# Kernel optimization log

Measured on AMD Instinct MI355X. Metric: run time of the kernel, lower is better.

Reference implementation:

```python
import jax, jax.numpy as jnp
import numpy as np

EMBED_DIM = 1024
NUM_HEADS = 16
HEAD_DIM = EMBED_DIM // NUM_HEADS
KERNEL = 3
PAD = KERNEL // 2
B, L = 4, 1024


def conv1d(x, w, b):
    # x: [B, D, L], w: [D_out, D_in, K], b: [D_out]; 'same' padding like nn.Conv1d(padding=K//2)
    y = jax.lax.conv_general_dilated(
        x, w, window_strides=(1,), padding=[(PAD, PAD)],
        dimension_numbers=('NCH', 'OIH', 'NCH'))
    return y + b[None, :, None]


def setup_inputs() -> dict:
    key = jax.random.key(0)
    ks = jax.random.split(key, 12)
    fan = EMBED_DIM * KERNEL
    bound = 1.0 / np.sqrt(fan)
    def wconv(k):
        return jax.random.uniform(k, (EMBED_DIM, EMBED_DIM, KERNEL), jnp.float32, -bound, bound)
    def bconv(k):
        return jax.random.uniform(k, (EMBED_DIM,), jnp.float32, -bound, bound)
    return {
        'query': jax.random.normal(ks[0], (B, L, EMBED_DIM), jnp.float32),
        'key': jax.random.normal(ks[1], (B, L, EMBED_DIM), jnp.float32),
        'value': jax.random.normal(ks[2], (B, L, EMBED_DIM), jnp.float32),
        'key_padding_mask': jax.random.randint(ks[3], (B, L), 0, 2) > 0,
        'attn_mask': jnp.zeros((L, L), jnp.float32),
        'q_w': wconv(ks[4]), 'q_b': bconv(ks[5]),
        'k_w': wconv(ks[6]), 'k_b': bconv(ks[7]),
        'v_w': wconv(ks[8]), 'v_b': bconv(ks[9]),
        'o_w': wconv(ks[10]), 'o_b': bconv(ks[11]),
    }


def reference(query, key, value, key_padding_mask, attn_mask,
              q_w, q_b, k_w, k_b, v_w, v_b, o_w, o_b):
    scale = HEAD_DIM ** -0.5
    # projections: [B, D, L]
    q = conv1d(jnp.swapaxes(query, 1, 2), q_w, q_b)
    k = conv1d(jnp.swapaxes(key, 1, 2), k_w, k_b)
    v = conv1d(jnp.swapaxes(value, 1, 2), v_w, v_b)
    # [B, H, d, L]
    q = q.reshape(B, NUM_HEADS, HEAD_DIM, L)
    k = k.reshape(B, NUM_HEADS, HEAD_DIM, L)
    v = v.reshape(B, NUM_HEADS, HEAD_DIM, L)
    # scores: [B, H, L, L]
    scores = jnp.einsum('bhdi,bhdj->bhij', q, k) * scale
    scores = scores + attn_mask[None, None, :, :]
    scores = jnp.where(key_padding_mask[:, None, None, :], -jnp.inf, scores)
    attn = jax.nn.softmax(scores, axis=-1)  # dropout p=0 (eval) -> identity
    out = jnp.einsum('bhij,bhdj->bhdi', attn, v)  # [B, H, d, L]
    out = out.reshape(B, EMBED_DIM, L)
    out = conv1d(out, o_w, o_b)
    return jnp.swapaxes(out, 1, 2)  # [B, L, D]
```

## Files before the change

kernel.cpp:

```cpp
#include <hip/hip_runtime.h>
#include <math.h>

#define NB 4
#define NL 1024
#define ND 1024
#define NH 16
#define HD 64

typedef __attribute__((ext_vector_type(8))) short bf16x8;
typedef __attribute__((ext_vector_type(4))) float f32x4;

static __device__ __forceinline__ unsigned short f32_to_bf16(float f) {
  unsigned u = __float_as_uint(f);
  u += 0x7FFFu + ((u >> 16) & 1u);
  return (unsigned short)(u >> 16);
}
static __device__ __forceinline__ float bf16_to_f32(unsigned short s) {
  return __uint_as_float(((unsigned)s) << 16);
}
static __device__ __forceinline__ void split1(float x, unsigned short* h, unsigned short* l) {
  unsigned u = __float_as_uint(x);
  *h = (unsigned short)(u >> 16);
  float r = x - __uint_as_float(u & 0xFFFF0000u);
  *l = (unsigned short)(__float_as_uint(r) >> 16);
}
static __device__ __forceinline__ void split8(float4 a, float4 b, bf16x8* hi, bf16x8* lo) {
  unsigned u[8] = {__float_as_uint(a.x), __float_as_uint(a.y),
                   __float_as_uint(a.z), __float_as_uint(a.w),
                   __float_as_uint(b.x), __float_as_uint(b.y),
                   __float_as_uint(b.z), __float_as_uint(b.w)};
  union { unsigned p[4]; bf16x8 v; } H, L;
#pragma unroll
  for (int p = 0; p < 4; ++p) {
    unsigned u0 = u[2 * p], u1 = u[2 * p + 1];
    H.p[p] = __builtin_amdgcn_perm(u1, u0, 0x07060302u);
    unsigned l0 = __float_as_uint(__uint_as_float(u0) - __uint_as_float(u0 & 0xFFFF0000u));
    unsigned l1 = __float_as_uint(__uint_as_float(u1) - __uint_as_float(u1 & 0xFFFF0000u));
    L.p[p] = __builtin_amdgcn_perm(l1, l0, 0x07060302u);
  }
  *hi = H.v; *lo = L.v;
}

__global__ __launch_bounds__(256) void wcvt_kernel(
    const float* __restrict__ w0, const float* __restrict__ w1,
    const float* __restrict__ w2, const float* __restrict__ w3,
    unsigned short* __restrict__ wb, int* __restrict__ flag)
{
  if (blockIdx.x == 0 && blockIdx.y == 0 && threadIdx.x == 0) flag[0] = 0;
  const int t = blockIdx.y;
  const int o = blockIdx.x;
  const float* w = (t == 0) ? w0 : (t == 1) ? w1 : (t == 2) ? w2 : w3;
  unsigned short* hi = wb + (size_t)t * 6 * (1u << 20);
  unsigned short* lo = hi + 3 * (1u << 20);
  const int tid = threadIdx.x;
  float v[12];
  const float* src = w + (size_t)o * (ND * 3) + tid * 12;
#pragma unroll
  for (int j = 0; j < 3; ++j) {
    float4 f = *(const float4*)(src + j * 4);
    v[j * 4 + 0] = f.x; v[j * 4 + 1] = f.y; v[j * 4 + 2] = f.z; v[j * 4 + 3] = f.w;
  }
#pragma unroll
  for (int k = 0; k < 3; ++k) {
    unsigned short hh[4], ll[4];
#pragma unroll
    for (int ii = 0; ii < 4; ++ii) {
      float x = v[ii * 3 + k];
      unsigned short h = f32_to_bf16(x);
      float r = x - bf16_to_f32(h);
      hh[ii] = h; ll[ii] = f32_to_bf16(r);
    }
    size_t dst = (size_t)k * (ND * ND) + (size_t)o * ND + tid * 4;
    *(ushort4*)&hi[dst] = make_ushort4(hh[0], hh[1], hh[2], hh[3]);
    *(ushort4*)&lo[dst] = make_ushort4(ll[0], ll[1], ll[2], ll[3]);
  }
}

__global__ __launch_bounds__(256) void amask_scan(
    const float* __restrict__ a, int* __restrict__ flag)
{
  size_t i = ((size_t)blockIdx.x * 256 + threadIdx.x) * 4;
  float4 v = *(const float4*)&a[i];
  if (v.x != 0.f || v.y != 0.f || v.z != 0.f || v.w != 0.f) atomicOr(flag, 1);
}

template <int MODE>
__global__ __launch_bounds__(256, 3) void conv_mfma5(
    const float* __restrict__ X0, const float* __restrict__ X1,
    const float* __restrict__ X2,
    const unsigned short* __restrict__ wb,
    const float* b0, const float* b1, const float* b2,
    unsigned short* qh, unsigned short* ql,
    unsigned short* kh, unsigned short* kl, unsigned short* vv,
    float* P)
{
  __shared__ __align__(16) float Af[4096];
  __shared__ __align__(16) unsigned short Bh[4096];
  __shared__ __align__(16) unsigned short Bl[4096];

  const int tid = threadIdx.x, lane = tid & 63, wave = tid >> 6;
  const int lin = blockIdx.x + 8 * (blockIdx.y + 32 * blockIdx.z);
  const int g = lin & 7, t = lin >> 3;
  const int nb = (g & 3) * 2 + (t & 1);
  const int mb = (g >> 2) * 16 + ((t >> 1) & 15);
  const int z  = t >> 5;
  const int n0 = nb * 128, m0 = mb * 128;
  const int b = m0 >> 10, l0v = m0 & (NL - 1);

  const unsigned short* Wh = (MODE == 0) ? wb + (size_t)z * 6 * (1u << 20) : wb;
  const unsigned short* Wl = Wh + 3 * (1u << 20);
  const float* X = (MODE == 0) ? (z == 0 ? X0 : (z == 1 ? X1 : X2)) : X0;

  const int wm = (wave >> 1) * 64, wn = (wave & 1) * 64;
  const int mrow = lane & 15, quad = lane >> 4;
  const int r16 = lane >> 2, cs = lane & 3;
  const int src_chunk = (cs - (r16 >> 1)) & 3;
  const int bswz = ((quad + (mrow >> 1)) & 3) * 8;

  f32x4 acc[4][4] = {};
  const int NS = (MODE == 0) ? 96 : 32;

  auto stage = [&](int s) {
    const int koff = (MODE == 0) ? (s >> 5) : z;
    const int i0 = (s & 31) * 32;
#pragma unroll
    for (int j = 0; j < 2; ++j) {
      const int seg = wave * 2 + j;
      const size_t gw = ((size_t)koff << 20) +
                        (size_t)(n0 + seg * 16 + r16) * ND + i0 + src_chunk * 8;
      __builtin_amdgcn_global_load_lds(
          (const __attribute__((address_space(1))) unsigned int*)(Wh + gw),
          (__attribute__((address_space(3))) unsigned int*)&Bh[seg * 512], 16, 0, 0);
      __builtin_amdgcn_global_load_lds(
          (const __attribute__((address_space(1))) unsigned int*)(Wl + gw),
          (__attribute__((address_space(3))) unsigned int*)&Bl[seg * 512], 16, 0, 0);
    }
#pragma unroll
    for (int j = 0; j < 4; ++j) {
      const int sl = (wave * 4 + j) * 64 + lane;
      const int row = sl >> 3, sir = sl & 7;
      const int chunk = (sir - (row & 7)) & 7;
      const float* gp;
      if (MODE == 0) {
        int l = l0v + row + koff - 1;
        l = (l < 0) ? 0 : (l > NL - 1 ? NL - 1 : l);
        gp = X + ((size_t)(b << 10) + l) * ND + i0 + chunk * 4;
      } else {
        gp = X + (size_t)(b * 1026 + l0v + z + row) * ND + i0 + chunk * 4;
      }
      __builtin_amdgcn_global_load_lds(
          (const __attribute__((address_space(1))) unsigned int*)gp,
          (__attribute__((address_space(3))) unsigned int*)&Af[(wave * 4 + j) * 256],
          16, 0, 0);
    }
  };

  bf16x8 ah[4], al[4], bh[4], bl[4];
  auto readfrags = [&]() {
#pragma unroll
    for (int mi = 0; mi < 4; ++mi) {
      const int row = wm + mi * 16 + mrow, r7 = row & 7;
      float4 fa = *(const float4*)&Af[row * 32 + (((quad * 2) + r7) & 7) * 4];
      float4 fb = *(const float4*)&Af[row * 32 + (((quad * 2 + 1) + r7) & 7) * 4];
      split8(fa, fb, &ah[mi], &al[mi]);
    }
#pragma unroll
    for (int ni = 0; ni < 4; ++ni) {
      const int brow = wn + ni * 16 + mrow;
      bh[ni] = *(const bf16x8*)&Bh[brow * 32 + bswz];
      bl[ni] = *(const bf16x8*)&Bl[brow * 32 + bswz];
    }
  };

  auto edgefix = [&](int s) {
    if (MODE == 0) {
      const int koff = s >> 5;
      const bool e_lo = (l0v == 0 && koff == 0);
      const bool e_hi = (l0v == NL - 128 && koff == 2);
      if (e_lo || e_hi) {
        const int er = e_lo ? 0 : 127;
        if (tid < 8) *(float4*)&Af[er * 32 + tid * 4] = make_float4(0.f, 0.f, 0.f, 0.f);
        __syncthreads();
      }
    }
  };

  stage(0);
  __syncthreads();
  edgefix(0);
  readfrags();

  for (int s = 0; s < NS; ++s) {
    __syncthreads();
    if (s + 1 < NS) stage(s + 1);
#pragma unroll
    for (int ni = 0; ni < 4; ++ni)
#pragma unroll
      for (int mi = 0; mi < 4; ++mi) {
        acc[mi][ni] = __builtin_amdgcn_mfma_f32_16x16x32_bf16(ah[mi], bh[ni], acc[mi][ni], 0, 0, 0);
        acc[mi][ni] = __builtin_amdgcn_mfma_f32_16x16x32_bf16(ah[mi], bl[ni], acc[mi][ni], 0, 0, 0);
        acc[mi][ni] = __builtin_amdgcn_mfma_f32_16x16x32_bf16(al[mi], bh[ni], acc[mi][ni], 0, 0, 0);
      }
    __syncthreads();
    if (s + 1 < NS) { edgefix(s + 1); readfrags(); }
  }

  if (MODE == 0) {
    const float* bias = (z == 0) ? b0 : (z == 1) ? b1 : b2;
#pragma unroll
    for (int ni = 0; ni < 4; ++ni) {
      const int n = n0 + wn + ni * 16 + mrow;
      const float bv = bias[n];
      const int h2 = n >> 6, dd = n & 63;
#pragma unroll
      for (int mi = 0; mi < 4; ++mi) {
        const int mbase = m0 + wm + mi * 16 + quad * 4;
        f32x4 v = acc[mi][ni];
#pragma unroll
        for (int r = 0; r < 4; ++r) {
          const int l = (mbase + r) & (NL - 1);
          const size_t o = (((size_t)b * NH + h2) * NL + l) * HD + dd;
          float val = v[r] + bv;
          if (z == 0) {
            val *= 0.125f;
            unsigned short hs, ls; split1(val, &hs, &ls);
            qh[o] = hs; ql[o] = ls;
          } else if (z == 1) {
            unsigned short hs, ls; split1(val, &hs, &ls);
            kh[o] = hs; kl[o] = ls;
          } else {
            vv[o] = f32_to_bf16(val);
          }
        }
      }
    }
  } else {
    float* Pz = P + (size_t)z * ((size_t)NB * NL * ND);
#pragma unroll
    for (int ni = 0; ni < 4; ++ni) {
      const int n = n0 + wn + ni * 16 + mrow;
#pragma unroll
      for (int mi = 0; mi < 4; ++mi) {
        const int mbase = m0 + wm + mi * 16 + quad * 4;
        f32x4 v = acc[mi][ni];
#pragma unroll
        for (int r = 0; r < 4; ++r) {
          const int l = (mbase + r) & (NL - 1);
          Pz[((size_t)(b << 10) + l) * ND + n] = v[r];
        }
      }
    }
  }
}

__global__ __launch_bounds__(256) void reduce_kernel(
    const float* __restrict__ P, const float* __restrict__ bias, float* __restrict__ out)
{
  const size_t S = (size_t)NB * NL * ND;
  const size_t idx = ((size_t)blockIdx.x * 256 + threadIdx.x) * 4;
  const int n = (int)(idx & (ND - 1));
  float4 p0 = *(const float4*)&P[idx];
  float4 p1 = *(const float4*)&P[idx + S];
  float4 p2 = *(const float4*)&P[idx + 2 * S];
  float4 bv = *(const float4*)&bias[n];
  float4 r;
  r.x = p0.x + p1.x + p2.x + bv.x;
  r.y = p0.y + p1.y + p2.y + bv.y;
  r.z = p0.z + p1.z + p2.z + bv.z;
  r.w = p0.w + p1.w + p2.w + bv.w;
  *(float4*)&out[idx] = r;
}

__global__ __launch_bounds__(256, 3) void attn_mfma3(
    const unsigned short* __restrict__ qhp, const unsigned short* __restrict__ qlp,
    const unsigned short* __restrict__ khp, const unsigned short* __restrict__ klp,
    const unsigned short* __restrict__ vvp, const int* __restrict__ kpm,
    const float* __restrict__ amask, const int* __restrict__ aflagp,
    float* __restrict__ AO)
{
  __shared__ __align__(16) unsigned short SM[8192 + 4608];
  unsigned short* Kh = SM;
  unsigned short* Kl = SM + 4096;
  unsigned short* Vt = SM + 8192;

  const int tid = threadIdx.x, lane = tid & 63, wave = tid >> 6;
  const int c = lane & 15, quad = lane >> 4;
  const int lin = blockIdx.x;
  const int bh_ = (lin & 7) + 8 * (lin >> 7);
  const int mt = (lin >> 3) & 15;
  const int b = bh_ >> 4, h = bh_ & 15;
  const int m0 = mt * 64;
  const size_t base = (size_t)bh_ * (NL * HD);
  const int aflag = *aflagp;
  const int mrow = wave * 16 + c;
  const int gm = m0 + mrow;

  if (h == 0 && mt == 0)
    *(float4*)&AO[(size_t)(b * 1026) * ND + tid * 4] = make_float4(0.f, 0.f, 0.f, 0.f);
  if (h == 0 && mt == 15)
    *(float4*)&AO[((size_t)(b * 1026) + 1025) * ND + tid * 4] = make_float4(0.f, 0.f, 0.f, 0.f);

  const int rowo = lane >> 3;
  const int grano = ((lane & 7) - rowo) & 7;

#pragma unroll
  for (int j = 0; j < 2; ++j) {
    const int s = wave * 2 + j;
    const size_t go = base + (size_t)(m0 + s * 8 + rowo) * HD + grano * 8;
    __builtin_amdgcn_global_load_lds(
        (const __attribute__((address_space(1))) unsigned int*)(qhp + go),
        (__attribute__((address_space(3))) unsigned int*)&Kh[s * 512], 16, 0, 0);
    __builtin_amdgcn_global_load_lds(
        (const __attribute__((address_space(1))) unsigned int*)(qlp + go),
        (__attribute__((address_space(3))) unsigned int*)&Kl[s * 512], 16, 0, 0);
  }
  __syncthreads();
  bf16x8 qbh[2], qbl[2];
#pragma unroll
  for (int kb = 0; kb < 2; ++kb) {
    const int cso = ((kb * 4 + quad + mrow) & 7) * 8;
    qbh[kb] = *(const bf16x8*)&Kh[mrow * 64 + cso];
    qbl[kb] = *(const bf16x8*)&Kl[mrow * 64 + cso];
  }

  f32x4 acc[4] = {};
  float m_r = -INFINITY, l_r = 0.0f;
  const int sr = tid >> 2, scq = tid & 3;

  for (int n0t = 0; n0t < NL; n0t += 64) {
    __syncthreads();

    float mval[4][4];
#pragma unroll
    for (int nf = 0; nf < 4; ++nf) {
      int4 pm4 = *(const int4*)&kpm[b * NL + n0t + nf * 16 + quad * 4];
      const int* pmi = &pm4.x;
#pragma unroll
      for (int r = 0; r < 4; ++r) {
        float am = 0.f;
        if (aflag) am = amask[(size_t)gm * NL + (n0t + nf * 16 + quad * 4 + r)];
        mval[nf][r] = pmi[r] ? -INFINITY : am;
      }
    }

#pragma unroll
    for (int j = 0; j < 2; ++j) {
      const int s = wave * 2 + j;
      const size_t go = base + (size_t)(n0t + s * 8 + rowo) * HD + grano * 8;
      __builtin_amdgcn_global_load_lds(
          (const __attribute__((address_space(1))) unsigned int*)(khp + go),
          (__attribute__((address_space(3))) unsigned int*)&Kh[s * 512], 16, 0, 0);
      __builtin_amdgcn_global_load_lds(
          (const __attribute__((address_space(1))) unsigned int*)(klp + go),
          (__attribute__((address_space(3))) unsigned int*)&Kl[s * 512], 16, 0, 0);
    }
#pragma unroll
    for (int ii = 0; ii < 2; ++ii) {
      const int c8 = scq * 2 + ii;
      uint4 u = *(const uint4*)(vvp + base + (size_t)(n0t + sr) * HD + c8 * 8);
      const unsigned short* pe = (const unsigned short*)&u;
#pragma unroll
      for (int e = 0; e < 8; ++e) {
        const int dd = c8 * 8 + e;
        Vt[dd * 72 + (((sr >> 3) + dd) & 7) * 8 + (sr & 7)] = pe[e];
      }
    }
    __syncthreads();

    f32x4 sa[4] = {};
#pragma unroll
    for (int kb = 0; kb < 2; ++kb)
#pragma unroll
      for (int nf = 0; nf < 4; ++nf) {
        const int row = nf * 16 + c;
        const int cso = ((kb * 4 + quad + row) & 7) * 8;
        bf16x8 kah = *(const bf16x8*)&Kh[row * 64 + cso];
        bf16x8 kal = *(const bf16x8*)&Kl[row * 64 + cso];
        sa[nf] = __builtin_amdgcn_mfma_f32_16x16x32_bf16(kah, qbh[kb], sa[nf], 0, 0, 0);
        sa[nf] = __builtin_amdgcn_mfma_f32_16x16x32_bf16(kah, qbl[kb], sa[nf], 0, 0, 0);
        sa[nf] = __builtin_amdgcn_mfma_f32_16x16x32_bf16(kal, qbh[kb], sa[nf], 0, 0, 0);
      }

    float p[4][4];
    float tmax = -INFINITY;
#pragma unroll
    for (int nf = 0; nf < 4; ++nf)
#pragma unroll
      for (int r = 0; r < 4; ++r) {
        float s = sa[nf][r] + mval[nf][r];
        p[nf][r] = s;
        tmax = fmaxf(tmax, s);
      }
    tmax = fmaxf(tmax, __shfl_xor(tmax, 16));
    tmax = fmaxf(tmax, __shfl_xor(tmax, 32));
    const float newm = fmaxf(m_r, tmax);
    const float msafe = (newm == -INFINITY) ? 0.f : newm;
    const float alpha = __expf(m_r - msafe);
    float rs = 0.f;
#pragma unroll
    for (int nf = 0; nf < 4; ++nf)
#pragma unroll
      for (int r = 0; r < 4; ++r) {
        float e = __expf(p[nf][r] - msafe);
        p[nf][r] = e;
        rs += e;
      }
    rs += __shfl_xor(rs, 16);
    rs += __shfl_xor(rs, 32);
    l_r = l_r * alpha + rs;
    m_r = newm;
#pragma unroll
    for (int df = 0; df < 4; ++df) {
      acc[df][0] *= alpha; acc[df][1] *= alpha;
      acc[df][2] *= alpha; acc[df][3] *= alpha;
    }

    unsigned q16[4][2];
#pragma unroll
    for (int nf = 0; nf < 4; ++nf)
#pragma unroll
      for (int w = 0; w < 2; ++w)
        q16[nf][w] = (unsigned)f32_to_bf16(p[nf][2 * w]) |
                     ((unsigned)f32_to_bf16(p[nf][2 * w + 1]) << 16);
#pragma unroll
    for (int kb = 0; kb < 2; ++kb) {
      union { unsigned d[4]; bf16x8 v; } pb;
#pragma unroll
      for (int w = 0; w < 4; ++w) {
        const int addr = ((((quad & 1) * 2 + (w >> 1)) * 16 + c) << 2);
        unsigned v0 = __builtin_amdgcn_ds_bpermute(addr, (int)q16[2 * kb][w & 1]);
        unsigned v1 = __builtin_amdgcn_ds_bpermute(addr, (int)q16[2 * kb + 1][w & 1]);
        pb.d[w] = (quad >> 1) ? v1 : v0;
      }
#pragma unroll
      for (int df = 0; df < 4; ++df) {
        const int row = df * 16 + c;
        const int cso = ((kb * 4 + quad + row) & 7) * 8;
        bf16x8 va = *(const bf16x8*)&Vt[row * 72 + cso];
        acc[df] = __builtin_amdgcn_mfma_f32_16x16x32_bf16(va, pb.v, acc[df], 0, 0, 0);
      }
    }
  }

  __syncthreads();
  const float inv = 1.0f / l_r;
  float* Ob = (float*)SM + wave * (16 * 68);
#pragma unroll
  for (int df = 0; df < 4; ++df)
#pragma unroll
    for (int r = 0; r < 4; ++r)
      Ob[c * 68 + df * 16 + quad * 4 + r] = acc[df][r] * inv;
  __syncthreads();
  const int mr2 = lane >> 2, cq2 = lane & 3;
#pragma unroll
  for (int ii = 0; ii < 4; ++ii) {
    const int chunk = cq2 * 4 + ii;
    float4 v = *(const float4*)&Ob[mr2 * 68 + chunk * 4];
    *(float4*)&AO[((size_t)(b * 1026) + (m0 + wave * 16 + mr2) + 1) * ND +
                  h * HD + chunk * 4] = v;
  }
}

extern "C" void kernel_launch(void* const* d_in, const int* in_sizes, int n_in,
                              void* d_out, int out_size, void* d_ws, size_t ws_size,
                              hipStream_t stream) {
  (void)in_sizes; (void)n_in; (void)out_size; (void)ws_size;
  const float* query = (const float*)d_in[0];
  const float* key_  = (const float*)d_in[1];
  const float* value = (const float*)d_in[2];
  const int*   kpm   = (const int*)d_in[3];
  const float* amask = (const float*)d_in[4];
  const float* q_w = (const float*)d_in[5];
  const float* q_b = (const float*)d_in[6];
  const float* k_w = (const float*)d_in[7];
  const float* k_b = (const float*)d_in[8];
  const float* v_w = (const float*)d_in[9];
  const float* v_b = (const float*)d_in[10];
  const float* o_w = (const float*)d_in[11];
  const float* o_b = (const float*)d_in[12];
  float* out = (float*)d_out;

  const size_t WB_BYTES = 50331648;
  unsigned short* Wb = (unsigned short*)d_ws;
  unsigned short* qh = (unsigned short*)((char*)d_ws + WB_BYTES);
  unsigned short* ql = qh + 4194304;
  unsigned short* kh = ql + 4194304;
  unsigned short* kl = kh + 4194304;
  unsigned short* vv = kl + 4194304;
  float* AO = (float*)d_ws;
  float* P  = (float*)((char*)d_ws + WB_BYTES);
  int* flag = (int*)d_out;

  wcvt_kernel<<<dim3(1024, 4), 256, 0, stream>>>(q_w, k_w, v_w, o_w, Wb, flag);
  amask_scan<<<1024, 256, 0, stream>>>(amask, flag);
  conv_mfma5<0><<<dim3(8, 32, 3), 256, 0, stream>>>(
      query, key_, value, Wb, q_b, k_b, v_b, qh, ql, kh, kl, vv, nullptr);
  attn_mfma3<<<1024, 256, 0, stream>>>(qh, ql, kh, kl, vv, kpm, amask, flag, AO);
  conv_mfma5<1><<<dim3(8, 32, 3), 256, 0, stream>>>(
      AO, nullptr, nullptr, Wb + (size_t)3 * 6 * (1u << 20),
      nullptr, nullptr, nullptr, nullptr, nullptr, nullptr, nullptr, nullptr, P);
  reduce_kernel<<<4096, 256, 0, stream>>>(P, o_b, out);
}
```

Baseline: 523.2 us.

## Switch conv GEMM to 32x32x16 MFMA and drop software prefetch of fragments

Replaces the 16x16x32 bf16 MFMA tiling in the conv projection kernel with 32x32x16 MFMA, so each wave holds a 2x2 grid of 32x32 accumulator tiles and issues fewer, larger instructions with fewer LDS fragment reads per FLOP. The loop is also restructured: it no longer stages the next K-slice while computing the current one, and instead loads, syncs, reads fragments and computes in sequence. The larger tiles are meant to cut LDS traffic and instruction overhead, but removing the overlap between global loads and MFMA work may expose memory latency. Epilogue index mapping is updated to the 32x32 accumulator layout.

```diff
diff --git a/kernel.cpp b/kernel.cpp
--- a/kernel.cpp
+++ b/kernel.cpp
@@ -9,6 +9,7 @@
 
 typedef __attribute__((ext_vector_type(8))) short bf16x8;
 typedef __attribute__((ext_vector_type(4))) float f32x4;
+typedef __attribute__((ext_vector_type(16))) float f32x16;
 
 static __device__ __forceinline__ unsigned short f32_to_bf16(float f) {
   unsigned u = __float_as_uint(f);
@@ -85,7 +86,7 @@
 }
 
 template <int MODE>
-__global__ __launch_bounds__(256, 3) void conv_mfma5(
+__global__ __launch_bounds__(256, 3) void conv_mfma6(
     const float* __restrict__ X0, const float* __restrict__ X1,
     const float* __restrict__ X2,
     const unsigned short* __restrict__ wb,
@@ -111,13 +112,12 @@
   const unsigned short* Wl = Wh + 3 * (1u << 20);
   const float* X = (MODE == 0) ? (z == 0 ? X0 : (z == 1 ? X1 : X2)) : X0;
 
-  const int wm = (wave >> 1) * 64, wn = (wave & 1) * 64;
-  const int mrow = lane & 15, quad = lane >> 4;
+  const int wm2 = (wave >> 1) * 64, wn2 = (wave & 1) * 64;
+  const int ln31 = lane & 31, khalf = lane >> 5;
   const int r16 = lane >> 2, cs = lane & 3;
   const int src_chunk = (cs - (r16 >> 1)) & 3;
-  const int bswz = ((quad + (mrow >> 1)) & 3) * 8;
-
-  f32x4 acc[4][4] = {};
+
+  f32x16 acc[2][2] = {};
   const int NS = (MODE == 0) ? 96 : 32;
 
   auto stage = [&](int s) {
@@ -155,23 +155,6 @@
     }
   };
 
-  bf16x8 ah[4], al[4], bh[4], bl[4];
-  auto readfrags = [&]() {
-#pragma unroll
-    for (int mi = 0; mi < 4; ++mi) {
-      const int row = wm + mi * 16 + mrow, r7 = row & 7;
-      float4 fa = *(const float4*)&Af[row * 32 + (((quad * 2) + r7) & 7) * 4];
-      float4 fb = *(const float4*)&Af[row * 32 + (((quad * 2 + 1) + r7) & 7) * 4];
-      split8(fa, fb, &ah[mi], &al[mi]);
-    }
-#pragma unroll
-    for (int ni = 0; ni < 4; ++ni) {
-      const int brow = wn + ni * 16 + mrow;
-      bh[ni] = *(const bf16x8*)&Bh[brow * 32 + bswz];
-      bl[ni] = *(const bf16x8*)&Bl[brow * 32 + bswz];
-    }
-  };
-
   auto edgefix = [&](int s) {
     if (MODE == 0) {
       const int koff = s >> 5;
@@ -185,42 +168,57 @@
     }
   };
 
-  stage(0);
-  __syncthreads();
-  edgefix(0);
-  readfrags();
-
   for (int s = 0; s < NS; ++s) {
+    stage(s);
     __syncthreads();
-    if (s + 1 < NS) stage(s + 1);
-#pragma unroll
-    for (int ni = 0; ni < 4; ++ni)
-#pragma unroll
-      for (int mi = 0; mi < 4; ++mi) {
-        acc[mi][ni] = __builtin_amdgcn_mfma_f32_16x16x32_bf16(ah[mi], bh[ni], acc[mi][ni], 0, 0, 0);
-        acc[mi][ni] = __builtin_amdgcn_mfma_f32_16x16x32_bf16(ah[mi], bl[ni], acc[mi][ni], 0, 0, 0);
-        acc[mi][ni] = __builtin_amdgcn_mfma_f32_16x16x32_bf16(al[mi], bh[ni], acc[mi][ni], 0, 0, 0);
+    edgefix(s);
+
+    bf16x8 ah[2][2], al[2][2];
+#pragma unroll
+    for (int mf = 0; mf < 2; ++mf) {
+      const int row = wm2 + mf * 32 + ln31, r7 = row & 7;
+#pragma unroll
+      for (int ts = 0; ts < 2; ++ts) {
+        const int c0 = ts * 4 + khalf * 2;
+        float4 fa = *(const float4*)&Af[row * 32 + (((c0 + 0) + r7) & 7) * 4];
+        float4 fb = *(const float4*)&Af[row * 32 + (((c0 + 1) + r7) & 7) * 4];
+        split8(fa, fb, &ah[mf][ts], &al[mf][ts]);
+      }
+    }
+#pragma unroll
+    for (int ts = 0; ts < 2; ++ts)
+#pragma unroll
+      for (int nf = 0; nf < 2; ++nf) {
+        const int brow = wn2 + nf * 32 + ln31;
+        const int slot = ((ts * 2 + khalf) + ((brow & 15) >> 1)) & 3;
+        bf16x8 bhf = *(const bf16x8*)&Bh[brow * 32 + slot * 8];
+        bf16x8 blf = *(const bf16x8*)&Bl[brow * 32 + slot * 8];
+#pragma unroll
+        for (int mf = 0; mf < 2; ++mf) {
+          acc[mf][nf] = __builtin_amdgcn_mfma_f32_32x32x16_bf16(ah[mf][ts], bhf, acc[mf][nf], 0, 0, 0);
+          acc[mf][nf] = __builtin_amdgcn_mfma_f32_32x32x16_bf16(ah[mf][ts], blf, acc[mf][nf], 0, 0, 0);
+          acc[mf][nf] = __builtin_amdgcn_mfma_f32_32x32x16_bf16(al[mf][ts], bhf, acc[mf][nf], 0, 0, 0);
+        }
       }
     __syncthreads();
-    if (s + 1 < NS) { edgefix(s + 1); readfrags(); }
   }
 
   if (MODE == 0) {
     const float* bias = (z == 0) ? b0 : (z == 1) ? b1 : b2;
 #pragma unroll
-    for (int ni = 0; ni < 4; ++ni) {
-      const int n = n0 + wn + ni * 16 + mrow;
+    for (int nf = 0; nf < 2; ++nf) {
+      const int n = n0 + wn2 + nf * 32 + ln31;
       const float bv = bias[n];
       const int h2 = n >> 6, dd = n & 63;
 #pragma unroll
-      for (int mi = 0; mi < 4; ++mi) {
-        const int mbase = m0 + wm + mi * 16 + quad * 4;
-        f32x4 v = acc[mi][ni];
-#pragma unroll
-        for (int r = 0; r < 4; ++r) {
-          const int l = (mbase + r) & (NL - 1);
+      for (int mf = 0; mf < 2; ++mf) {
+        f32x16 v = acc[mf][nf];
+#pragma unroll
+        for (int reg = 0; reg < 16; ++reg) {
+          const int mloc = (reg & 3) + 8 * (reg >> 2) + 4 * khalf;
+          const int l = l0v + wm2 + mf * 32 + mloc;
           const size_t o = (((size_t)b * NH + h2) * NL + l) * HD + dd;
-          float val = v[r] + bv;
+          float val = v[reg] + bv;
           if (z == 0) {
             val *= 0.125f;
             unsigned short hs, ls; split1(val, &hs, &ls);
@@ -237,16 +235,16 @@
   } else {
     float* Pz = P + (size_t)z * ((size_t)NB * NL * ND);
 #pragma unroll
-    for (int ni = 0; ni < 4; ++ni) {
-      const int n = n0 + wn + ni * 16 + mrow;
-#pragma unroll
-      for (int mi = 0; mi < 4; ++mi) {
-        const int mbase = m0 + wm + mi * 16 + quad * 4;
-        f32x4 v = acc[mi][ni];
-#pragma unroll
-        for (int r = 0; r < 4; ++r) {
-          const int l = (mbase + r) & (NL - 1);
-          Pz[((size_t)(b << 10) + l) * ND + n] = v[r];
+    for (int nf = 0; nf < 2; ++nf) {
+      const int n = n0 + wn2 + nf * 32 + ln31;
+#pragma unroll
+      for (int mf = 0; mf < 2; ++mf) {
+        f32x16 v = acc[mf][nf];
+#pragma unroll
+        for (int reg = 0; reg < 16; ++reg) {
+          const int mloc = (reg & 3) + 8 * (reg >> 2) + 4 * khalf;
+          const int l = l0v + wm2 + mf * 32 + mloc;
+          Pz[((size_t)(b << 10) + l) * ND + n] = v[reg];
         }
       }
     }
@@ -493,10 +491,10 @@
 
   wcvt_kernel<<<dim3(1024, 4), 256, 0, stream>>>(q_w, k_w, v_w, o_w, Wb, flag);
   amask_scan<<<1024, 256, 0, stream>>>(amask, flag);
-  conv_mfma5<0><<<dim3(8, 32, 3), 256, 0, stream>>>(
+  conv_mfma6<0><<<dim3(8, 32, 3), 256, 0, stream>>>(
       query, key_, value, Wb, q_b, k_b, v_b, qh, ql, kh, kl, vv, nullptr);
   attn_mfma3<<<1024, 256, 0, stream>>>(qh, ql, kh, kl, vv, kpm, amask, flag, AO);
-  conv_mfma5<1><<<dim3(8, 32, 3), 256, 0, stream>>>(
+  conv_mfma6<1><<<dim3(8, 32, 3), 256, 0, stream>>>(
       AO, nullptr, nullptr, Wb + (size_t)3 * 6 * (1u << 20),
       nullptr, nullptr, nullptr, nullptr, nullptr, nullptr, nullptr, nullptr, P);
   reduce_kernel<<<4096, 256, 0, stream>>>(P, o_b, out);
```

Result: slower. 534.9 us (+2.2%).

## Store V transposed from projection and DMA it directly in attention

Applied to the files above, without the earlier changes.

The projection epilogue now writes V in a [B,H,d,L] transposed layout with packed 4-wide stores. The attention kernel can then load V tiles straight into LDS with global_load_lds instead of transposing them element by element through registers. The conv kernel's software prefetch and fragment preload are also removed in favour of a simpler load-sync-compute loop, which lowers register pressure but exposes load latency. The swizzle used when reading V from LDS relies on the new DMA placement matching the old XOR pattern.

```diff
diff --git a/kernel.cpp b/kernel.cpp
--- a/kernel.cpp
+++ b/kernel.cpp
@@ -85,13 +85,13 @@
 }
 
 template <int MODE>
-__global__ __launch_bounds__(256, 3) void conv_mfma5(
+__global__ __launch_bounds__(256, 3) void conv_mfma7(
     const float* __restrict__ X0, const float* __restrict__ X1,
     const float* __restrict__ X2,
     const unsigned short* __restrict__ wb,
     const float* b0, const float* b1, const float* b2,
     unsigned short* qh, unsigned short* ql,
-    unsigned short* kh, unsigned short* kl, unsigned short* vv,
+    unsigned short* kh, unsigned short* kl, unsigned short* vt,
     float* P)
 {
   __shared__ __align__(16) float Af[4096];
@@ -120,7 +120,7 @@
   f32x4 acc[4][4] = {};
   const int NS = (MODE == 0) ? 96 : 32;
 
-  auto stage = [&](int s) {
+  for (int s = 0; s < NS; ++s) {
     const int koff = (MODE == 0) ? (s >> 5) : z;
     const int i0 = (s & 31) * 32;
 #pragma unroll
@@ -153,28 +153,8 @@
           (__attribute__((address_space(3))) unsigned int*)&Af[(wave * 4 + j) * 256],
           16, 0, 0);
     }
-  };
-
-  bf16x8 ah[4], al[4], bh[4], bl[4];
-  auto readfrags = [&]() {
-#pragma unroll
-    for (int mi = 0; mi < 4; ++mi) {
-      const int row = wm + mi * 16 + mrow, r7 = row & 7;
-      float4 fa = *(const float4*)&Af[row * 32 + (((quad * 2) + r7) & 7) * 4];
-      float4 fb = *(const float4*)&Af[row * 32 + (((quad * 2 + 1) + r7) & 7) * 4];
-      split8(fa, fb, &ah[mi], &al[mi]);
-    }
-#pragma unroll
-    for (int ni = 0; ni < 4; ++ni) {
-      const int brow = wn + ni * 16 + mrow;
-      bh[ni] = *(const bf16x8*)&Bh[brow * 32 + bswz];
-      bl[ni] = *(const bf16x8*)&Bl[brow * 32 + bswz];
-    }
-  };
-
-  auto edgefix = [&](int s) {
+    __syncthreads();
     if (MODE == 0) {
-      const int koff = s >> 5;
       const bool e_lo = (l0v == 0 && koff == 0);
       const bool e_hi = (l0v == NL - 128 && koff == 2);
       if (e_lo || e_hi) {
@@ -183,26 +163,27 @@
         __syncthreads();
       }
     }
-  };
-
-  stage(0);
-  __syncthreads();
-  edgefix(0);
-  readfrags();
-
-  for (int s = 0; s < NS; ++s) {
+    bf16x8 ah[4], al[4];
+#pragma unroll
+    for (int mi = 0; mi < 4; ++mi) {
+      const int row = wm + mi * 16 + mrow, r7 = row & 7;
+      float4 fa = *(const float4*)&Af[row * 32 + (((quad * 2) + r7) & 7) * 4];
+      float4 fb = *(const float4*)&Af[row * 32 + (((quad * 2 + 1) + r7) & 7) * 4];
+      split8(fa, fb, &ah[mi], &al[mi]);
+    }
+#pragma unroll
+    for (int ni = 0; ni < 4; ++ni) {
+      const int brow = wn + ni * 16 + mrow;
+      bf16x8 bh = *(const bf16x8*)&Bh[brow * 32 + bswz];
+      bf16x8 bl = *(const bf16x8*)&Bl[brow * 32 + bswz];
+#pragma unroll
+      for (int mi = 0; mi < 4; ++mi) {
+        acc[mi][ni] = __builtin_amdgcn_mfma_f32_16x16x32_bf16(ah[mi], bh, acc[mi][ni], 0, 0, 0);
+        acc[mi][ni] = __builtin_amdgcn_mfma_f32_16x16x32_bf16(ah[mi], bl, acc[mi][ni], 0, 0, 0);
+        acc[mi][ni] = __builtin_amdgcn_mfma_f32_16x16x32_bf16(al[mi], bh, acc[mi][ni], 0, 0, 0);
+      }
+    }
     __syncthreads();
-    if (s + 1 < NS) stage(s + 1);
-#pragma unroll
-    for (int ni = 0; ni < 4; ++ni)
-#pragma unroll
-      for (int mi = 0; mi < 4; ++mi) {
-        acc[mi][ni] = __builtin_amdgcn_mfma_f32_16x16x32_bf16(ah[mi], bh[ni], acc[mi][ni], 0, 0, 0);
-        acc[mi][ni] = __builtin_amdgcn_mfma_f32_16x16x32_bf16(ah[mi], bl[ni], acc[mi][ni], 0, 0, 0);
-        acc[mi][ni] = __builtin_amdgcn_mfma_f32_16x16x32_bf16(al[mi], bh[ni], acc[mi][ni], 0, 0, 0);
-      }
-    __syncthreads();
-    if (s + 1 < NS) { edgefix(s + 1); readfrags(); }
   }
 
   if (MODE == 0) {
@@ -215,21 +196,26 @@
 #pragma unroll
       for (int mi = 0; mi < 4; ++mi) {
         const int mbase = m0 + wm + mi * 16 + quad * 4;
+        const int lb = mbase & (NL - 1);
         f32x4 v = acc[mi][ni];
-#pragma unroll
-        for (int r = 0; r < 4; ++r) {
-          const int l = (mbase + r) & (NL - 1);
-          const size_t o = (((size_t)b * NH + h2) * NL + l) * HD + dd;
-          float val = v[r] + bv;
-          if (z == 0) {
-            val *= 0.125f;
-            unsigned short hs, ls; split1(val, &hs, &ls);
-            qh[o] = hs; ql[o] = ls;
-          } else if (z == 1) {
-            unsigned short hs, ls; split1(val, &hs, &ls);
-            kh[o] = hs; kl[o] = ls;
-          } else {
-            vv[o] = f32_to_bf16(val);
+        if (z == 2) {
+          ushort4 pk;
+          pk.x = f32_to_bf16(v[0] + bv); pk.y = f32_to_bf16(v[1] + bv);
+          pk.z = f32_to_bf16(v[2] + bv); pk.w = f32_to_bf16(v[3] + bv);
+          *(ushort4*)&vt[(((size_t)b * NH + h2) * HD + dd) * NL + lb] = pk;
+        } else {
+#pragma unroll
+          for (int r = 0; r < 4; ++r) {
+            const size_t o = (((size_t)b * NH + h2) * NL + (lb + r)) * HD + dd;
+            float val = v[r] + bv;
+            if (z == 0) {
+              val *= 0.125f;
+              unsigned short hs, ls; split1(val, &hs, &ls);
+              qh[o] = hs; ql[o] = ls;
+            } else {
+              unsigned short hs, ls; split1(val, &hs, &ls);
+              kh[o] = hs; kl[o] = ls;
+            }
           }
         }
       }
@@ -271,14 +257,14 @@
   *(float4*)&out[idx] = r;
 }
 
-__global__ __launch_bounds__(256, 3) void attn_mfma3(
+__global__ __launch_bounds__(256, 3) void attn_mfma4(
     const unsigned short* __restrict__ qhp, const unsigned short* __restrict__ qlp,
     const unsigned short* __restrict__ khp, const unsigned short* __restrict__ klp,
-    const unsigned short* __restrict__ vvp, const int* __restrict__ kpm,
+    const unsigned short* __restrict__ vtp, const int* __restrict__ kpm,
     const float* __restrict__ amask, const int* __restrict__ aflagp,
     float* __restrict__ AO)
 {
-  __shared__ __align__(16) unsigned short SM[8192 + 4608];
+  __shared__ __align__(16) unsigned short SM[3 * 4096];
   unsigned short* Kh = SM;
   unsigned short* Kl = SM + 4096;
   unsigned short* Vt = SM + 8192;
@@ -291,6 +277,7 @@
   const int b = bh_ >> 4, h = bh_ & 15;
   const int m0 = mt * 64;
   const size_t base = (size_t)bh_ * (NL * HD);
+  const size_t vbase = (size_t)bh_ * (HD * NL);
   const int aflag = *aflagp;
   const int mrow = wave * 16 + c;
   const int gm = m0 + mrow;
@@ -325,7 +312,6 @@
 
   f32x4 acc[4] = {};
   float m_r = -INFINITY, l_r = 0.0f;
-  const int sr = tid >> 2, scq = tid & 3;
 
   for (int n0t = 0; n0t < NL; n0t += 64) {
     __syncthreads();
@@ -353,17 +339,10 @@
       __builtin_amdgcn_global_load_lds(
           (const __attribute__((address_space(1))) unsigned int*)(klp + go),
           (__attribute__((address_space(3))) unsigned int*)&Kl[s * 512], 16, 0, 0);
-    }
-#pragma unroll
-    for (int ii = 0; ii < 2; ++ii) {
-      const int c8 = scq * 2 + ii;
-      uint4 u = *(const uint4*)(vvp + base + (size_t)(n0t + sr) * HD + c8 * 8);
-      const unsigned short* pe = (const unsigned short*)&u;
-#pragma unroll
-      for (int e = 0; e < 8; ++e) {
-        const int dd = c8 * 8 + e;
-        Vt[dd * 72 + (((sr >> 3) + dd) & 7) * 8 + (sr & 7)] = pe[e];
-      }
+      const size_t gv = vbase + (size_t)(s * 8 + rowo) * NL + n0t + grano * 8;
+      __builtin_amdgcn_global_load_lds(
+          (const __attribute__((address_space(1))) unsigned int*)(vtp + gv),
+          (__attribute__((address_space(3))) unsigned int*)&Vt[s * 512], 16, 0, 0);
     }
     __syncthreads();
 
@@ -436,7 +415,7 @@
       for (int df = 0; df < 4; ++df) {
         const int row = df * 16 + c;
         const int cso = ((kb * 4 + quad + row) & 7) * 8;
-        bf16x8 va = *(const bf16x8*)&Vt[row * 72 + cso];
+        bf16x8 va = *(const bf16x8*)&Vt[row * 64 + cso];
         acc[df] = __builtin_amdgcn_mfma_f32_16x16x32_bf16(va, pb.v, acc[df], 0, 0, 0);
       }
     }
@@ -486,17 +465,17 @@
   unsigned short* ql = qh + 4194304;
   unsigned short* kh = ql + 4194304;
   unsigned short* kl = kh + 4194304;
-  unsigned short* vv = kl + 4194304;
+  unsigned short* vt = kl + 4194304;
   float* AO = (float*)d_ws;
   float* P  = (float*)((char*)d_ws + WB_BYTES);
   int* flag = (int*)d_out;
 
   wcvt_kernel<<<dim3(1024, 4), 256, 0, stream>>>(q_w, k_w, v_w, o_w, Wb, flag);
   amask_scan<<<1024, 256, 0, stream>>>(amask, flag);
-  conv_mfma5<0><<<dim3(8, 32, 3), 256, 0, stream>>>(
-      query, key_, value, Wb, q_b, k_b, v_b, qh, ql, kh, kl, vv, nullptr);
-  attn_mfma3<<<1024, 256, 0, stream>>>(qh, ql, kh, kl, vv, kpm, amask, flag, AO);
-  conv_mfma5<1><<<dim3(8, 32, 3), 256, 0, stream>>>(
+  conv_mfma7<0><<<dim3(8, 32, 3), 256, 0, stream>>>(
+      query, key_, value, Wb, q_b, k_b, v_b, qh, ql, kh, kl, vt, nullptr);
+  attn_mfma4<<<1024, 256, 0, stream>>>(qh, ql, kh, kl, vt, kpm, amask, flag, AO);
+  conv_mfma7<1><<<dim3(8, 32, 3), 256, 0, stream>>>(
       AO, nullptr, nullptr, Wb + (size_t)3 * 6 * (1u << 20),
       nullptr, nullptr, nullptr, nullptr, nullptr, nullptr, nullptr, nullptr, P);
   reduce_kernel<<<4096, 256, 0, stream>>>(P, o_b, out);
```

Result: faster. 511.9 us (-2.2%).
